# Kernel optimization log

Hardware: AMD Instinct MI355X
Metric: run time of the kernel (lower is better)

Reference implementation:

```python
import jax, jax.numpy as jnp
import numpy as np

NUM_IMG = 3          # num_image_channels
NUM_HID = 16         # num_hidden_channels
NUM_OUT = 1          # num_output_channels
C = NUM_IMG + NUM_HID + NUM_OUT   # 20 total channels
NFILT = 2            # num_learned_filters
HIDDEN = 128         # hidden_size
FIRE_RATE = 0.5
KS = 3               # kernel_size


def setup_inputs() -> dict:
    key = jax.random.key(0)
    ks = jax.random.split(key, 6)
    B, H, W = 8, 256, 256
    x = jax.random.normal(ks[0], (B, C, H, W), dtype=jnp.float32)
    # learned depthwise perception filters, shape [C, 1, 3, 3] (OIHW, groups=C)
    w_f1 = jax.random.normal(ks[1], (C, 1, KS, KS), dtype=jnp.float32) * 0.1
    w_f2 = jax.random.normal(ks[2], (C, 1, KS, KS), dtype=jnp.float32) * 0.1
    # pointwise MLP: Conv2d(60->128, 1x1, bias) ; Conv2d(128->20, 1x1, no bias)
    in_vec = C * (NFILT + 1)  # 60
    W1 = jax.random.normal(ks[3], (HIDDEN, in_vec), dtype=jnp.float32) * (1.0 / np.sqrt(in_vec))
    b1 = jax.random.normal(ks[4], (HIDDEN,), dtype=jnp.float32) * 0.01
    # torch inits this to zero; use small random so gradients/outputs are non-trivial
    W2 = jax.random.normal(ks[5], (C, HIDDEN), dtype=jnp.float32) * 0.02
    return {"x": x, "w_f1": w_f1, "w_f2": w_f2, "W1": W1, "b1": b1, "W2": W2, "steps": 4}


def _dwconv_reflect(x, w):
    # depthwise 3x3 conv with reflect padding (padding_mode='reflect', padding=1)
    xp = jnp.pad(x, ((0, 0), (0, 0), (1, 1), (1, 1)), mode='reflect')
    return jax.lax.conv_general_dilated(
        xp, w, window_strides=(1, 1), padding='VALID',
        feature_group_count=C,
        dimension_numbers=('NCHW', 'OIHW', 'NCHW'))


def reference(x, w_f1, w_f2, W1, b1, W2, steps):
    # channel mask: image channels are immutable (dx zeroed there)
    ch_mask = (jnp.arange(C) >= NUM_IMG).astype(x.dtype)[None, :, None, None]
    base_key = jax.random.key(42)
    B, _, H, W = x.shape
    for step in range(steps):
        # perceive: concat [x, f1(x), f2(x)] -> [B, 3C, H, W]
        perc = jnp.concatenate([x, _dwconv_reflect(x, w_f1), _dwconv_reflect(x, w_f2)], axis=1)
        # pointwise MLP (1x1 convs)
        h = jax.nn.relu(jnp.einsum('oc,bchw->bohw', W1, perc) + b1[None, :, None, None])
        dx = jnp.einsum('oc,bchw->bohw', W2, h)
        # stochastic fire-rate mask, shared across channels
        k = jax.random.fold_in(base_key, step)
        stoch = (jax.random.uniform(k, (B, 1, H, W)) < FIRE_RATE).astype(x.dtype)
        x = x + dx * stoch * ch_mask
    return x
```

## Files before the change

kernel.cpp:

```cpp
#include <hip/hip_runtime.h>
#include <stdint.h>


#define Bsz 8
#define Cn  20
#define Hn  256
#define Wn  256
#define HW  (Hn*Wn)

typedef float  f32x4  __attribute__((ext_vector_type(4)));
typedef __bf16 bf16x8 __attribute__((ext_vector_type(8)));
typedef __bf16 bf16x4 __attribute__((ext_vector_type(4)));
typedef short  s16x8  __attribute__((ext_vector_type(8)));

__device__ __bf16 g_W1p[128 * 64];
__device__ __bf16 g_W2p[2 * 4 * 64 * 8];
__device__ float  g_wf1[Cn * 9];
__device__ float  g_wf2[Cn * 9];

__device__ __host__ __forceinline__ void tf2x32(uint32_t k0, uint32_t k1,
                                                uint32_t x0, uint32_t x1,
                                                uint32_t& o0, uint32_t& o1) {
  uint32_t ks2 = k0 ^ k1 ^ 0x1BD11BDAu;
  x0 += k0; x1 += k1;
#define TFR(r) { x0 += x1; x1 = (x1 << (r)) | (x1 >> (32 - (r))); x1 ^= x0; }
  TFR(13) TFR(15) TFR(26) TFR(6)
  x0 += k1;  x1 += ks2 + 1u;
  TFR(17) TFR(29) TFR(16) TFR(24)
  x0 += ks2; x1 += k0 + 2u;
  TFR(13) TFR(15) TFR(26) TFR(6)
  x0 += k0;  x1 += k1 + 3u;
  TFR(17) TFR(29) TFR(16) TFR(24)
  x0 += k1;  x1 += ks2 + 4u;
  TFR(13) TFR(15) TFR(26) TFR(6)
  x0 += ks2; x1 += k0 + 5u;
#undef TFR
  o0 = x0; o1 = x1;
}

__device__ __forceinline__ f32x4 mfma16(bf16x8 a, bf16x8 b, f32x4 c) {
  return __builtin_amdgcn_mfma_f32_16x16x32_bf16(
      __builtin_bit_cast(s16x8, a), __builtin_bit_cast(s16x8, b), c, 0, 0, 0);
}

__global__ void pack_weights(const float* __restrict__ W1, const float* __restrict__ W2,
                             const float* __restrict__ wf1, const float* __restrict__ wf2) {
  int t = blockIdx.x * 256 + threadIdx.x;
  for (int i = t; i < 128 * 64; i += gridDim.x * 256) {
    int e = i & 7, l = (i >> 3) & 63, kb = (i >> 9) & 1, nt = (i >> 10) & 1, ch = i >> 11;
    int j = ch * 32 + nt * 16 + (l & 15);
    int k = kb * 32 + (l >> 4) * 8 + e;
    g_W1p[i] = (k < 60) ? (__bf16)W1[j * 60 + k] : (__bf16)0.f;
  }
  for (int i = t; i < 2 * 4 * 64 * 8; i += gridDim.x * 256) {
    int e = i & 7, l = (i >> 3) & 63, kb = (i >> 9) & 3, mt = (i >> 11) & 1;
    int ch = mt * 16 + (l & 15);
    int j  = kb * 32 + (l >> 4) * 8 + e;
    g_W2p[i] = (ch >= 3 && ch < Cn) ? (__bf16)W2[ch * 128 + j] : (__bf16)0.f;
  }
  for (int i = t; i < Cn * 9; i += gridDim.x * 256) {
    g_wf1[i] = wf1[i];
    g_wf2[i] = wf2[i];
  }
}

template <int SIN, int SOUT>
__global__ __launch_bounds__(256, 4) void nca_step(
    const float* __restrict__ src, float* __restrict__ dst,
    const float* __restrict__ b1, uint32_t ka, uint32_t kb_key) {

  __shared__ __align__(16) __bf16 smem[4 * 2560];

  const int tid = threadIdx.x;
  const int w = tid >> 6, l = tid & 63;
  __bf16* lds = smem + w * 2560;

  const int lin = (blockIdx.z * 16 + blockIdx.y) * 16 + blockIdx.x;
  const int swzb = (lin & 7) * 256 + (lin >> 3);
  const int b  = swzb >> 8;
  const int by = ((swzb >> 4) & 15) * 16;
  const int bx = (swzb & 15) * 16;
  const int by0 = by + (w >> 1) * 8;
  const int bx0 = bx + (w & 1) * 8;

#pragma unroll
  for (int s = 0; s < 2; ++s) {
    int h = l + s * 64;
    if (h < 100) {
      int hy = h / 10, hx = h - hy * 10;
      int gy = by0 - 1 + hy; gy = (gy < 0) ? -gy : ((gy >= Hn) ? 2 * Hn - 2 - gy : gy);
      int gx = bx0 - 1 + hx; gx = (gx < 0) ? -gx : ((gx >= Wn) ? 2 * Wn - 2 - gx : gx);
      const int idx = gy * Wn + gx;
      bf16x8 q0, q1; bf16x4 q2;
      if constexpr (SIN == 0) {
        const float* sp = src + (size_t)b * Cn * HW + idx;
#pragma unroll
        for (int c = 0; c < 8; ++c)  q0[c] = (__bf16)sp[(size_t)c * HW];
#pragma unroll
        for (int c = 0; c < 8; ++c)  q1[c] = (__bf16)sp[(size_t)(c + 8) * HW];
#pragma unroll
        for (int c = 0; c < 4; ++c)  q2[c] = (__bf16)sp[(size_t)(c + 16) * HW];
      } else {
        const f32x4* pb = (const f32x4*)src;
        f32x4 v0 = pb[(0 * Bsz + b) * HW + idx];
        f32x4 v1 = pb[(1 * Bsz + b) * HW + idx];
        f32x4 v2 = pb[(2 * Bsz + b) * HW + idx];
        f32x4 v3 = pb[(3 * Bsz + b) * HW + idx];
        f32x4 v4 = pb[(4 * Bsz + b) * HW + idx];
#pragma unroll
        for (int c = 0; c < 4; ++c) { q0[c] = (__bf16)v0[c]; q0[c + 4] = (__bf16)v1[c]; }
#pragma unroll
        for (int c = 0; c < 4; ++c) { q1[c] = (__bf16)v2[c]; q1[c + 4] = (__bf16)v3[c]; }
#pragma unroll
        for (int c = 0; c < 4; ++c)  q2[c] = (__bf16)v4[c];
      }
      __bf16* wp = lds + h * 24;
      *(bf16x8*)(wp)      = q0;
      *(bf16x8*)(wp + 8)  = q1;
      *(bf16x4*)(wp + 16) = q2;
    }
  }

  const int py = l >> 3, px_ = l & 7;
  uint32_t y0, y1;
  tf2x32(ka, kb_key, 0u, (uint32_t)((b * Hn + by0 + py) * Wn + bx0 + px_), y0, y1);
  const unsigned long long fmask = __ballot(((y0 ^ y1) & 0x80000000u) == 0u);

  float a1[Cn], a2[Cn];
#pragma unroll
  for (int c = 0; c < Cn; ++c) { a1[c] = 0.f; a2[c] = 0.f; }
  bf16x8 id0, id1; bf16x4 id2;

#pragma unroll
  for (int ky = 0; ky < 3; ++ky)
#pragma unroll
    for (int kx = 0; kx < 3; ++kx) {
      const __bf16* tp = lds + ((py + ky) * 10 + px_ + kx) * 24;
      bf16x8 t0 = *(const bf16x8*)(tp);
      bf16x8 t1 = *(const bf16x8*)(tp + 8);
      bf16x4 t2 = *(const bf16x4*)(tp + 16);
      if (ky == 1 && kx == 1) { id0 = t0; id1 = t1; id2 = t2; }
      const int tap = ky * 3 + kx;
#pragma unroll
      for (int c = 0; c < 8; ++c) {
        float v = (float)t0[c];
        a1[c] = fmaf(g_wf1[c * 9 + tap], v, a1[c]);
        a2[c] = fmaf(g_wf2[c * 9 + tap], v, a2[c]);
      }
#pragma unroll
      for (int c = 0; c < 8; ++c) {
        float v = (float)t1[c];
        a1[c + 8] = fmaf(g_wf1[(c + 8) * 9 + tap], v, a1[c + 8]);
        a2[c + 8] = fmaf(g_wf2[(c + 8) * 9 + tap], v, a2[c + 8]);
      }
#pragma unroll
      for (int c = 0; c < 4; ++c) {
        float v = (float)t2[c];
        a1[c + 16] = fmaf(g_wf1[(c + 16) * 9 + tap], v, a1[c + 16]);
        a2[c + 16] = fmaf(g_wf2[(c + 16) * 9 + tap], v, a2[c + 16]);
      }
    }

  const int g4 = l >> 4, c16 = l & 15;

  bf16x8 af[4][2];
#pragma unroll
  for (int kb = 0; kb < 2; ++kb) {
#pragma unroll
    for (int g2 = 0; g2 < 4; ++g2) {
      bf16x8 pk;
#pragma unroll
      for (int e = 0; e < 8; ++e) {
        const int k = kb * 32 + g2 * 8 + e;
        __bf16 v;
        if      (k < 8)  v = id0[k];
        else if (k < 16) v = id1[k - 8];
        else if (k < 20) v = id2[k - 16];
        else if (k < 40) v = (__bf16)a1[k - 20];
        else if (k < 60) v = (__bf16)a2[k - 40];
        else             v = (__bf16)0.f;
        pk[e] = v;
      }
      *(bf16x8*)(lds + l * 40 + g2 * 8) = pk;
    }
#pragma unroll
    for (int mt = 0; mt < 4; ++mt)
      af[mt][kb] = *(const bf16x8*)(lds + (mt * 16 + c16) * 40 + g4 * 8);
  }

  const f32x4 zero4 = {0.f, 0.f, 0.f, 0.f};
  f32x4 acc2[2][4];
#pragma unroll
  for (int mt = 0; mt < 2; ++mt)
#pragma unroll
    for (int nt = 0; nt < 4; ++nt) acc2[mt][nt] = zero4;

  const bf16x8* w1v = (const bf16x8*)g_W1p;
  const bf16x8* w2v = (const bf16x8*)g_W2p;

  for (int ch4 = 0; ch4 < 4; ++ch4) {
#pragma unroll
    for (int nt = 0; nt < 2; ++nt) {
      bf16x8 bw0 = w1v[((ch4 * 2 + nt) * 2 + 0) * 64 + l];
      bf16x8 bw1 = w1v[((ch4 * 2 + nt) * 2 + 1) * 64 + l];
      const float bias = b1[ch4 * 32 + nt * 16 + c16];
#pragma unroll
      for (int mt = 0; mt < 4; ++mt) {
        f32x4 a = mfma16(af[mt][0], bw0, zero4);
        a = mfma16(af[mt][1], bw1, a);
#pragma unroll
        for (int r = 0; r < 4; ++r) {
          float hv = fmaxf(a[r] + bias, 0.f);
          lds[(mt * 16 + g4 * 4 + r) * 40 + nt * 16 + c16] = (__bf16)hv;
        }
      }
    }
    bf16x8 wa0 = w2v[(0 * 4 + ch4) * 64 + l];
    bf16x8 wa1 = w2v[(1 * 4 + ch4) * 64 + l];
#pragma unroll
    for (int nt = 0; nt < 4; ++nt) {
      bf16x8 hb = *(const bf16x8*)(lds + (nt * 16 + c16) * 40 + g4 * 8);
      acc2[0][nt] = mfma16(wa0, hb, acc2[0][nt]);
      acc2[1][nt] = mfma16(wa1, hb, acc2[1][nt]);
    }
  }

  if constexpr (SOUT == 1) {
    float* ldsf = (float*)lds;
#pragma unroll
    for (int nt = 0; nt < 4; ++nt) {
      const int px = nt * 16 + c16;
      *(f32x4*)(ldsf + px * 20 + g4 * 4) = acc2[0][nt];
      if (g4 == 0) *(f32x4*)(ldsf + px * 20 + 16) = acc2[1][nt];
    }
    const int idx = (by0 + py) * Wn + (bx0 + px_);
    const float fire = ((fmask >> l) & 1ull) ? 1.f : 0.f;
    f32x4* db = (f32x4*)dst;
#pragma unroll
    for (int p = 0; p < 5; ++p) {
      f32x4 dxv = *(const f32x4*)(ldsf + l * 20 + p * 4);
      f32x4 xv;
      if constexpr (SIN == 0) {
        const float* sp = src + (size_t)b * Cn * HW + idx;
#pragma unroll
        for (int r = 0; r < 4; ++r) xv[r] = sp[(size_t)(p * 4 + r) * HW];
      } else {
        xv = ((const f32x4*)src)[(p * Bsz + b) * HW + idx];
      }
      f32x4 ov;
#pragma unroll
      for (int r = 0; r < 4; ++r) ov[r] = xv[r] + dxv[r] * fire;
      db[(p * Bsz + b) * HW + idx] = ov;
    }
  } else {
    float* __restrict__ ob = dst + (size_t)b * Cn * HW;
#pragma unroll
    for (int nt = 0; nt < 4; ++nt) {
      const int pxl = nt * 16 + c16;
      const int gy = by0 + (pxl >> 3), gx = bx0 + (pxl & 7);
      const size_t pix = (size_t)gy * Wn + gx;
      const float fire = ((fmask >> pxl) & 1ull) ? 1.f : 0.f;
#pragma unroll
      for (int mt = 0; mt < 2; ++mt) {
        if (mt == 0 || g4 == 0) {
          f32x4 xv = ((const f32x4*)src)[((mt * 4 + g4) * Bsz + b) * HW + pix];
#pragma unroll
          for (int r = 0; r < 4; ++r) {
            const int ch = mt * 16 + g4 * 4 + r;
            ob[(size_t)ch * HW + pix] = xv[r] + acc2[mt][nt][r] * fire;
          }
        }
      }
    }
  }
}

extern "C" void kernel_launch(void* const* d_in, const int* in_sizes, int n_in,
                              void* d_out, int out_size, void* d_ws, size_t ws_size,
                              hipStream_t stream) {
  const float* x   = (const float*)d_in[0];
  const float* wf1 = (const float*)d_in[1];
  const float* wf2 = (const float*)d_in[2];
  const float* W1  = (const float*)d_in[3];
  const float* b1  = (const float*)d_in[4];
  const float* W2  = (const float*)d_in[5];

  float* out = (float*)d_out;
  float* ws0 = (float*)d_ws;

  pack_weights<<<8, 256, 0, stream>>>(W1, W2, wf1, wf2);

  dim3 grid(16, 16, Bsz);
  dim3 blk(256);

  uint32_t ka, kb;
  tf2x32(0u, 42u, 0u, 0u, ka, kb);
  nca_step<0, 1><<<grid, blk, 0, stream>>>(x,   ws0, b1, ka, kb);
  tf2x32(0u, 42u, 0u, 1u, ka, kb);
  nca_step<1, 1><<<grid, blk, 0, stream>>>(ws0, out, b1, ka, kb);
  tf2x32(0u, 42u, 0u, 2u, ka, kb);
  nca_step<1, 1><<<grid, blk, 0, stream>>>(out, ws0, b1, ka, kb);
  tf2x32(0u, 42u, 0u, 3u, ka, kb);
  nca_step<1, 0><<<grid, blk, 0, stream>>>(ws0, out, b1, ka, kb);
}
```

Baseline: 151.6 us.

## Use 4x64 block tiles with shared halo and swap MFMA operands

Each block now covers a 4-row by 64-column strip instead of four separate 8x8 wave tiles. The whole block loads one shared 6x66 halo into LDS behind a __syncthreads, and each wave works on one full row of 64 pixels. This makes global reads longer and contiguous per row, and the loaded halo is shared across the block instead of each wave loading its own. The first MLP layer now passes W1 as the A operand, so the hidden activations can be written to LDS as vectorized bf16x4 stores, and the bias is read as a vector load. The costs are a block-wide barrier and more LDS per block, which may limit occupancy.

```diff
diff --git a/kernel.cpp b/kernel.cpp
--- a/kernel.cpp
+++ b/kernel.cpp
@@ -47,15 +47,15 @@
                              const float* __restrict__ wf1, const float* __restrict__ wf2) {
   int t = blockIdx.x * 256 + threadIdx.x;
   for (int i = t; i < 128 * 64; i += gridDim.x * 256) {
-    int e = i & 7, l = (i >> 3) & 63, kb = (i >> 9) & 1, nt = (i >> 10) & 1, ch = i >> 11;
-    int j = ch * 32 + nt * 16 + (l & 15);
+    int e = i & 7, l = (i >> 3) & 63, kb = (i >> 9) & 1, jt = (i >> 10) & 1, q = i >> 11;
+    int j = q * 32 + jt * 16 + (l & 15);
     int k = kb * 32 + (l >> 4) * 8 + e;
     g_W1p[i] = (k < 60) ? (__bf16)W1[j * 60 + k] : (__bf16)0.f;
   }
-  for (int i = t; i < 2 * 4 * 64 * 8; i += gridDim.x * 256) {
-    int e = i & 7, l = (i >> 3) & 63, kb = (i >> 9) & 3, mt = (i >> 11) & 1;
+  for (int i = t; i < 2 * 4 * 512; i += gridDim.x * 256) {
+    int e = i & 7, l = (i >> 3) & 63, q = (i >> 9) & 3, mt = i >> 11;
     int ch = mt * 16 + (l & 15);
-    int j  = kb * 32 + (l >> 4) * 8 + e;
+    int j  = q * 32 + (l >> 4) * 8 + e;
     g_W2p[i] = (ch >= 3 && ch < Cn) ? (__bf16)W2[ch * 128 + j] : (__bf16)0.f;
   }
   for (int i = t; i < Cn * 9; i += gridDim.x * 256) {
@@ -69,62 +69,60 @@
     const float* __restrict__ src, float* __restrict__ dst,
     const float* __restrict__ b1, uint32_t ka, uint32_t kb_key) {
 
-  __shared__ __align__(16) __bf16 smem[4 * 2560];
+  __shared__ __align__(16) __bf16 halo[6 * 66 * 24];
+  __shared__ __align__(16) __bf16 r1all[4 * 2560];
 
   const int tid = threadIdx.x;
   const int w = tid >> 6, l = tid & 63;
-  __bf16* lds = smem + w * 2560;
-
-  const int lin = (blockIdx.z * 16 + blockIdx.y) * 16 + blockIdx.x;
+  __bf16* r1 = r1all + w * 2560;
+
+  const int lin = (blockIdx.z * 64 + blockIdx.y) * 4 + blockIdx.x;
   const int swzb = (lin & 7) * 256 + (lin >> 3);
-  const int b  = swzb >> 8;
-  const int by = ((swzb >> 4) & 15) * 16;
-  const int bx = (swzb & 15) * 16;
-  const int by0 = by + (w >> 1) * 8;
-  const int bx0 = bx + (w & 1) * 8;
-
-#pragma unroll
-  for (int s = 0; s < 2; ++s) {
-    int h = l + s * 64;
-    if (h < 100) {
-      int hy = h / 10, hx = h - hy * 10;
-      int gy = by0 - 1 + hy; gy = (gy < 0) ? -gy : ((gy >= Hn) ? 2 * Hn - 2 - gy : gy);
-      int gx = bx0 - 1 + hx; gx = (gx < 0) ? -gx : ((gx >= Wn) ? 2 * Wn - 2 - gx : gx);
-      const int idx = gy * Wn + gx;
-      bf16x8 q0, q1; bf16x4 q2;
-      if constexpr (SIN == 0) {
-        const float* sp = src + (size_t)b * Cn * HW + idx;
-#pragma unroll
-        for (int c = 0; c < 8; ++c)  q0[c] = (__bf16)sp[(size_t)c * HW];
-#pragma unroll
-        for (int c = 0; c < 8; ++c)  q1[c] = (__bf16)sp[(size_t)(c + 8) * HW];
-#pragma unroll
-        for (int c = 0; c < 4; ++c)  q2[c] = (__bf16)sp[(size_t)(c + 16) * HW];
-      } else {
-        const f32x4* pb = (const f32x4*)src;
-        f32x4 v0 = pb[(0 * Bsz + b) * HW + idx];
-        f32x4 v1 = pb[(1 * Bsz + b) * HW + idx];
-        f32x4 v2 = pb[(2 * Bsz + b) * HW + idx];
-        f32x4 v3 = pb[(3 * Bsz + b) * HW + idx];
-        f32x4 v4 = pb[(4 * Bsz + b) * HW + idx];
-#pragma unroll
-        for (int c = 0; c < 4; ++c) { q0[c] = (__bf16)v0[c]; q0[c + 4] = (__bf16)v1[c]; }
-#pragma unroll
-        for (int c = 0; c < 4; ++c) { q1[c] = (__bf16)v2[c]; q1[c + 4] = (__bf16)v3[c]; }
-#pragma unroll
-        for (int c = 0; c < 4; ++c)  q2[c] = (__bf16)v4[c];
-      }
-      __bf16* wp = lds + h * 24;
-      *(bf16x8*)(wp)      = q0;
-      *(bf16x8*)(wp + 8)  = q1;
-      *(bf16x4*)(wp + 16) = q2;
-    }
-  }
-
-  const int py = l >> 3, px_ = l & 7;
+  const int b   = swzb >> 8;
+  const int rem = swzb & 255;
+  const int by0 = (rem >> 2) * 4;
+  const int bx0 = (rem & 3) * 64;
+
+  for (int t = tid; t < 6 * 66; t += 256) {
+    int ry = t / 66, cx = t - ry * 66;
+    int gy = by0 - 1 + ry; gy = (gy < 0) ? -gy : ((gy >= Hn) ? 2 * Hn - 2 - gy : gy);
+    int gx = bx0 - 1 + cx; gx = (gx < 0) ? -gx : ((gx >= Wn) ? 2 * Wn - 2 - gx : gx);
+    const int idx = gy * Wn + gx;
+    bf16x8 q0, q1; bf16x4 q2;
+    if constexpr (SIN == 0) {
+      const float* sp = src + (size_t)b * Cn * HW + idx;
+#pragma unroll
+      for (int c = 0; c < 8; ++c)  q0[c] = (__bf16)sp[(size_t)c * HW];
+#pragma unroll
+      for (int c = 0; c < 8; ++c)  q1[c] = (__bf16)sp[(size_t)(c + 8) * HW];
+#pragma unroll
+      for (int c = 0; c < 4; ++c)  q2[c] = (__bf16)sp[(size_t)(c + 16) * HW];
+    } else {
+      const f32x4* pb = (const f32x4*)src;
+      f32x4 v0 = pb[(0 * Bsz + b) * HW + idx];
+      f32x4 v1 = pb[(1 * Bsz + b) * HW + idx];
+      f32x4 v2 = pb[(2 * Bsz + b) * HW + idx];
+      f32x4 v3 = pb[(3 * Bsz + b) * HW + idx];
+      f32x4 v4 = pb[(4 * Bsz + b) * HW + idx];
+#pragma unroll
+      for (int c = 0; c < 4; ++c) { q0[c] = (__bf16)v0[c]; q0[c + 4] = (__bf16)v1[c]; }
+#pragma unroll
+      for (int c = 0; c < 4; ++c) { q1[c] = (__bf16)v2[c]; q1[c + 4] = (__bf16)v3[c]; }
+#pragma unroll
+      for (int c = 0; c < 4; ++c)  q2[c] = (__bf16)v4[c];
+    }
+    __bf16* wp = halo + t * 24;
+    *(bf16x8*)(wp)      = q0;
+    *(bf16x8*)(wp + 8)  = q1;
+    *(bf16x4*)(wp + 16) = q2;
+  }
+
+  const int gy = by0 + w;
   uint32_t y0, y1;
-  tf2x32(ka, kb_key, 0u, (uint32_t)((b * Hn + by0 + py) * Wn + bx0 + px_), y0, y1);
+  tf2x32(ka, kb_key, 0u, (uint32_t)((b * Hn + gy) * Wn + bx0 + l), y0, y1);
   const unsigned long long fmask = __ballot(((y0 ^ y1) & 0x80000000u) == 0u);
+
+  __syncthreads();
 
   float a1[Cn], a2[Cn];
 #pragma unroll
@@ -135,7 +133,7 @@
   for (int ky = 0; ky < 3; ++ky)
 #pragma unroll
     for (int kx = 0; kx < 3; ++kx) {
-      const __bf16* tp = lds + ((py + ky) * 10 + px_ + kx) * 24;
+      const __bf16* tp = halo + ((w + ky) * 66 + l + kx) * 24;
       bf16x8 t0 = *(const bf16x8*)(tp);
       bf16x8 t1 = *(const bf16x8*)(tp + 8);
       bf16x4 t2 = *(const bf16x4*)(tp + 16);
@@ -181,11 +179,11 @@
         else             v = (__bf16)0.f;
         pk[e] = v;
       }
-      *(bf16x8*)(lds + l * 40 + g2 * 8) = pk;
-    }
-#pragma unroll
-    for (int mt = 0; mt < 4; ++mt)
-      af[mt][kb] = *(const bf16x8*)(lds + (mt * 16 + c16) * 40 + g4 * 8);
+      *(bf16x8*)(r1 + l * 40 + g2 * 8) = pk;
+    }
+#pragma unroll
+    for (int pxt = 0; pxt < 4; ++pxt)
+      af[pxt][kb] = *(const bf16x8*)(r1 + (pxt * 16 + c16) * 40 + g4 * 8);
   }
 
   const f32x4 zero4 = {0.f, 0.f, 0.f, 0.f};
@@ -198,42 +196,42 @@
   const bf16x8* w1v = (const bf16x8*)g_W1p;
   const bf16x8* w2v = (const bf16x8*)g_W2p;
 
-  for (int ch4 = 0; ch4 < 4; ++ch4) {
-#pragma unroll
-    for (int nt = 0; nt < 2; ++nt) {
-      bf16x8 bw0 = w1v[((ch4 * 2 + nt) * 2 + 0) * 64 + l];
-      bf16x8 bw1 = w1v[((ch4 * 2 + nt) * 2 + 1) * 64 + l];
-      const float bias = b1[ch4 * 32 + nt * 16 + c16];
-#pragma unroll
-      for (int mt = 0; mt < 4; ++mt) {
-        f32x4 a = mfma16(af[mt][0], bw0, zero4);
-        a = mfma16(af[mt][1], bw1, a);
-#pragma unroll
-        for (int r = 0; r < 4; ++r) {
-          float hv = fmaxf(a[r] + bias, 0.f);
-          lds[(mt * 16 + g4 * 4 + r) * 40 + nt * 16 + c16] = (__bf16)hv;
-        }
-      }
-    }
-    bf16x8 wa0 = w2v[(0 * 4 + ch4) * 64 + l];
-    bf16x8 wa1 = w2v[(1 * 4 + ch4) * 64 + l];
+  for (int q = 0; q < 4; ++q) {
+#pragma unroll
+    for (int jt = 0; jt < 2; ++jt) {
+      bf16x8 aw0 = w1v[((q * 2 + jt) * 2 + 0) * 64 + l];
+      bf16x8 aw1 = w1v[((q * 2 + jt) * 2 + 1) * 64 + l];
+      const f32x4 bias = *(const f32x4*)(b1 + q * 32 + jt * 16 + g4 * 4);
+#pragma unroll
+      for (int pxt = 0; pxt < 4; ++pxt) {
+        f32x4 a = mfma16(aw0, af[pxt][0], zero4);
+        a = mfma16(aw1, af[pxt][1], a);
+        bf16x4 hv;
+#pragma unroll
+        for (int r = 0; r < 4; ++r)
+          hv[r] = (__bf16)fmaxf(a[r] + bias[r], 0.f);
+        *(bf16x4*)(r1 + (pxt * 16 + c16) * 40 + jt * 16 + g4 * 4) = hv;
+      }
+    }
+    bf16x8 wa0 = w2v[(0 * 4 + q) * 64 + l];
+    bf16x8 wa1 = w2v[(1 * 4 + q) * 64 + l];
 #pragma unroll
     for (int nt = 0; nt < 4; ++nt) {
-      bf16x8 hb = *(const bf16x8*)(lds + (nt * 16 + c16) * 40 + g4 * 8);
+      bf16x8 hb = *(const bf16x8*)(r1 + (nt * 16 + c16) * 40 + g4 * 8);
       acc2[0][nt] = mfma16(wa0, hb, acc2[0][nt]);
       acc2[1][nt] = mfma16(wa1, hb, acc2[1][nt]);
     }
   }
 
   if constexpr (SOUT == 1) {
-    float* ldsf = (float*)lds;
+    float* ldsf = (float*)r1;
 #pragma unroll
     for (int nt = 0; nt < 4; ++nt) {
       const int px = nt * 16 + c16;
       *(f32x4*)(ldsf + px * 20 + g4 * 4) = acc2[0][nt];
       if (g4 == 0) *(f32x4*)(ldsf + px * 20 + 16) = acc2[1][nt];
     }
-    const int idx = (by0 + py) * Wn + (bx0 + px_);
+    const int idx = gy * Wn + bx0 + l;
     const float fire = ((fmask >> l) & 1ull) ? 1.f : 0.f;
     f32x4* db = (f32x4*)dst;
 #pragma unroll
@@ -257,8 +255,7 @@
 #pragma unroll
     for (int nt = 0; nt < 4; ++nt) {
       const int pxl = nt * 16 + c16;
-      const int gy = by0 + (pxl >> 3), gx = bx0 + (pxl & 7);
-      const size_t pix = (size_t)gy * Wn + gx;
+      const size_t pix = (size_t)gy * Wn + bx0 + pxl;
       const float fire = ((fmask >> pxl) & 1ull) ? 1.f : 0.f;
 #pragma unroll
       for (int mt = 0; mt < 2; ++mt) {
@@ -290,7 +287,7 @@
 
   pack_weights<<<8, 256, 0, stream>>>(W1, W2, wf1, wf2);
 
-  dim3 grid(16, 16, Bsz);
+  dim3 grid(4, 64, Bsz);
   dim3 blk(256);
 
   uint32_t ka, kb;
```

Result: faster. 143.6 us (median of 4 runs) (-5.3%).
